# Kernel optimization log

Measured on AMD Instinct MI355X. Metric: run time of the kernel, lower is better.

The kernel has to match this reference:

```python
import jax, jax.numpy as jnp
import numpy as np

NUM_HEADS = 8  # matches init_kwargs

def setup_inputs() -> dict:
    key = jax.random.key(0)
    ks = jax.random.split(key, 5)
    b, n, c = 8, 4096, 512
    scale_in = 1.0 / np.sqrt(c)
    return {
        'x': jax.random.normal(ks[0], (b, n, c), jnp.float32),
        'wqkv_w': jax.random.normal(ks[1], (3 * c, c), jnp.float32) * scale_in,
        'wqkv_b': jax.random.normal(ks[2], (3 * c,), jnp.float32) * 0.02,
        'wp_w': jax.random.normal(ks[3], (c, c), jnp.float32) * scale_in,
        'wp_b': jax.random.normal(ks[4], (c,), jnp.float32) * 0.02,
    }

def reference(x, wqkv_w, wqkv_b, wp_w, wp_b):
    b, n, c = x.shape
    h = NUM_HEADS
    d = c // h
    # QKV projection (torch Linear: x @ W^T + b)
    qkv = x @ wqkv_w.T + wqkv_b                      # (b, n, 3c)
    qkv = jnp.transpose(qkv.reshape(b, n, 3, c), (2, 0, 1, 3))
    q, k, v = qkv[0], qkv[1], qkv[2]                 # each (b, n, c)
    # Faithful to original: reshape (b,n,h,d) -> (b,h,n,d) is a FLAT
    # reinterpretation (torch .reshape), not a transpose.
    q = q.reshape(b, n, h, d).reshape(b, h, n, d)
    k = k.reshape(b, n, h, d).reshape(b, h, n, d)
    v = v.reshape(b, n, h, d).reshape(b, h, n, d)
    # Channel (cross-covariance) attention: contract over tokens n.
    scores = jnp.einsum('bhnd,bhne->bhde', q, k) / jnp.sqrt(jnp.float32(d))
    weights = jax.nn.softmax(scores, axis=-1)        # softmax over head_dim
    y = jnp.einsum('bhde,bhme->bhdm', weights, v)    # (b, h, d, n)
    y = jnp.transpose(y, (0, 3, 1, 2)).reshape(b, n, c)
    return y @ wp_w.T + wp_b
```

## Files before the change

kernel.cpp:

```cpp
#include <hip/hip_runtime.h>

typedef short s16x8 __attribute__((ext_vector_type(8)));
typedef float f32x4 __attribute__((ext_vector_type(4)));
typedef unsigned short us;

__device__ inline us f2bf(float f){
    union{float f;unsigned u;} v{f};
    unsigned r = v.u + 0x7fff + ((v.u>>16)&1);
    return (us)(r>>16);
}
__device__ inline float bf2f(us h){
    union{unsigned u;float f;} v{(unsigned)h<<16};
    return v.f;
}

__device__ __forceinline__ void glds16(const us* g, us* l){
    __builtin_amdgcn_global_load_lds(
        (const __attribute__((address_space(1))) unsigned int*)(g),
        (__attribute__((address_space(3))) unsigned int*)(l), 16, 0, 0);
}

__global__ void cast_f32_bf16(const float* __restrict__ src, us* __restrict__ dst, int n4){
    int i = blockIdx.x*blockDim.x + threadIdx.x;
    if(i < n4){
        float4 f = ((const float4*)src)[i];
        ushort4 o;
        o.x = f2bf(f.x); o.y = f2bf(f.y); o.z = f2bf(f.z); o.w = f2bf(f.w);
        ((ushort4*)dst)[i] = o;
    }
}

template<int BF16OUT>
__launch_bounds__(256,2)
__global__ void gemm_bt(const us* __restrict__ A, const us* __restrict__ B,
                        const float* __restrict__ bias, void* __restrict__ Cv,
                        int M, int N, int K){
    __shared__ __attribute__((aligned(16))) us sA[128*32];
    __shared__ __attribute__((aligned(16))) us sB[128*32];
    int t = threadIdx.x;
    int bm = blockIdx.y, bn = blockIdx.x;
    int lane = t & 63, wave = t >> 6;
    int quad = lane >> 4, l15 = lane & 15;
    int wm = wave >> 1, wn = wave & 1;

    int srow = wave*32 + (lane>>2);
    int scol = (lane&3)*8;
    const us* Ag = A + (size_t)(bm*128 + srow)*K + scol;
    const us* Bg = B + (size_t)(bn*128 + srow)*K + scol;
    us* sAw = &sA[(wave*32)*32];
    us* sBw = &sB[(wave*32)*32];

    f32x4 acc[4][4];
    #pragma unroll
    for(int i=0;i<4;i++)
        #pragma unroll
        for(int j=0;j<4;j++) acc[i][j] = (f32x4){0.f,0.f,0.f,0.f};

    for(int k0=0; k0<K; k0+=32){
        glds16(Ag + k0,                sAw);
        glds16(Ag + (size_t)16*K + k0, sAw + 16*32);
        glds16(Bg + k0,                sBw);
        glds16(Bg + (size_t)16*K + k0, sBw + 16*32);
        __syncthreads();
        s16x8 af[4], bfr[4];
        #pragma unroll
        for(int i=0;i<4;i++) af[i]  = *(const s16x8*)&sA[(wm*64 + i*16 + l15)*32 + quad*8];
        #pragma unroll
        for(int j=0;j<4;j++) bfr[j] = *(const s16x8*)&sB[(wn*64 + j*16 + l15)*32 + quad*8];
        #pragma unroll
        for(int i=0;i<4;i++)
            #pragma unroll
            for(int j=0;j<4;j++)
                acc[i][j] = __builtin_amdgcn_mfma_f32_16x16x32_bf16(af[i], bfr[j], acc[i][j], 0,0,0);
        __syncthreads();
    }

    int row0 = bm*128 + wm*64;
    int col0 = bn*128 + wn*64;
    #pragma unroll
    for(int j=0;j<4;j++){
        int col = col0 + j*16 + l15;
        float bv = bias[col];
        #pragma unroll
        for(int i=0;i<4;i++){
            int rbase = row0 + i*16 + quad*4;
            #pragma unroll
            for(int r=0;r<4;r++){
                float v = acc[i][j][r] + bv;
                if(BF16OUT) ((us*)Cv)[(size_t)(rbase+r)*N + col] = f2bf(v);
                else        ((float*)Cv)[(size_t)(rbase+r)*N + col] = v;
            }
        }
    }
}

__launch_bounds__(256,2)
__global__ void attn_scores_mfma(const us* __restrict__ qkv, float* __restrict__ Sp){
    __shared__ __attribute__((aligned(16))) us sQt[64*64];
    __shared__ __attribute__((aligned(16))) us sKt[64*64];
    int t = threadIdx.x;
    int kb = blockIdx.x, head = blockIdx.y;
    int lane = t & 63, w = t >> 6;
    int quad = lane >> 4, l15 = lane & 15;

    f32x4 acc[4];
    #pragma unroll
    for(int j=0;j<4;j++) acc[j] = (f32x4){0.f,0.f,0.f,0.f};

    for(int chunk=0; chunk<8; chunk++){
        int r0 = head*512 + kb*64 + chunk*8;
        #pragma unroll
        for(int it=0; it<2; it++){
            int i = it*256 + t;
            int row8 = i>>6, l = i&63;
            int d0 = (l&7)*8;
            int off = ((row8 ^ (l&7))<<3) | (l>>3);
            const us* gq = qkv + (size_t)(r0+row8)*1536 + l*8;
            union{uint4 v; us s[8];} q, k;
            q.v = *(const uint4*)gq;
            k.v = *(const uint4*)(gq + 512);
            #pragma unroll
            for(int j=0;j<8;j++){
                sQt[(d0+j)*64 + off] = q.s[j];
                sKt[(d0+j)*64 + off] = k.s[j];
            }
        }
        __syncthreads();
        #pragma unroll
        for(int ks=0; ks<2; ks++){
            int d = w*16 + l15;
            int tb = ks*4 + quad;
            s16x8 af = *(const s16x8*)&sQt[d*64 + ((tb ^ (d>>3))<<3)];
            #pragma unroll
            for(int jt=0; jt<4; jt++){
                int e = jt*16 + l15;
                s16x8 bf = *(const s16x8*)&sKt[e*64 + ((tb ^ (e>>3))<<3)];
                acc[jt] = __builtin_amdgcn_mfma_f32_16x16x32_bf16(af, bf, acc[jt], 0,0,0);
            }
        }
        __syncthreads();
    }

    float* S = Sp + (size_t)(kb*64 + head)*4096;
    #pragma unroll
    for(int jt=0; jt<4; jt++){
        int e = jt*16 + l15;
        #pragma unroll
        for(int r=0; r<4; r++){
            int d = w*16 + quad*4 + r;
            S[d*64 + e] = acc[jt][r];
        }
    }
}

__global__ void softmax_fuse(const float* __restrict__ Sp, us* __restrict__ W){
    int head = blockIdx.x;
    int t = threadIdx.x;
    int d = t>>2, eg = (t&3)*16;
    float v[16];
    #pragma unroll
    for(int e=0;e<16;e++) v[e]=0.f;
    for(int kb=0; kb<8; kb++){
        const float* p = Sp + (size_t)(kb*64 + head)*4096 + d*64 + eg;
        #pragma unroll
        for(int e4=0;e4<4;e4++){
            float4 f = ((const float4*)p)[e4];
            v[e4*4+0]+=f.x; v[e4*4+1]+=f.y; v[e4*4+2]+=f.z; v[e4*4+3]+=f.w;
        }
    }
    float m = -1e30f;
    #pragma unroll
    for(int e=0;e<16;e++){ v[e] *= 0.125f; m = fmaxf(m, v[e]); }
    m = fmaxf(m, __shfl_xor(m, 1));
    m = fmaxf(m, __shfl_xor(m, 2));
    float s = 0.f;
    #pragma unroll
    for(int e=0;e<16;e++){ v[e] = __expf(v[e]-m); s += v[e]; }
    s += __shfl_xor(s, 1);
    s += __shfl_xor(s, 2);
    float inv = 1.f/s;
    union{uint4 u[2]; us h[16];} o;
    #pragma unroll
    for(int e=0;e<16;e++) o.h[e] = f2bf(v[e]*inv);
    uint4* wp = (uint4*)(W + (size_t)head*4096 + d*64 + eg);
    wp[0] = o.u[0]; wp[1] = o.u[1];
}

__launch_bounds__(256,2)
__global__ void attn_pv(const us* __restrict__ qkv, const us* __restrict__ W,
                        us* __restrict__ attn){
    const int LV = 72;
    __shared__ __attribute__((aligned(16))) us sV[128*72];
    __shared__ __attribute__((aligned(16))) us sW[64*72];
    int t = threadIdx.x;
    int head = blockIdx.y, chunk = blockIdx.x;
    int rbase = head*512;
    #pragma unroll
    for(int it=0; it<4; it++){
        int i = it*2048 + t*8;
        int tok = i>>6, e = i&63;
        int qrow = i>>9, ch = i&511;
        *(uint4*)&sV[tok*LV + e] = *(const uint4*)&qkv[(size_t)(rbase + chunk*16 + qrow)*1536 + 1024 + ch];
    }
    #pragma unroll
    for(int it=0; it<2; it++){
        int i = it*2048 + t*8;
        int dd = i>>6, e = i&63;
        *(uint4*)&sW[dd*LV + e] = *(const uint4*)&W[head*4096 + i];
    }
    __syncthreads();
    int lane = t&63, w = t>>6, quad = lane>>4, l15 = lane&15;
    f32x4 acc[2][4];
    #pragma unroll
    for(int i=0;i<2;i++)
        #pragma unroll
        for(int j=0;j<4;j++) acc[i][j] = (f32x4){0.f,0.f,0.f,0.f};
    #pragma unroll
    for(int ks=0; ks<2; ks++){
        int k0 = ks*32;
        s16x8 af[2], bfr[4];
        #pragma unroll
        for(int mt=0;mt<2;mt++) af[mt]  = *(const s16x8*)&sV[(w*32+mt*16+l15)*LV + k0 + quad*8];
        #pragma unroll
        for(int nt=0;nt<4;nt++) bfr[nt] = *(const s16x8*)&sW[(nt*16+l15)*LV + k0 + quad*8];
        #pragma unroll
        for(int mt=0;mt<2;mt++)
            #pragma unroll
            for(int nt=0;nt<4;nt++)
                acc[mt][nt] = __builtin_amdgcn_mfma_f32_16x16x32_bf16(af[mt], bfr[nt], acc[mt][nt],0,0,0);
    }
    int b = head>>3, h = head&7;
    #pragma unroll
    for(int mt=0;mt<2;mt++){
        int mg = chunk*128 + w*32 + mt*16 + quad*4;
        #pragma unroll
        for(int nt=0;nt<4;nt++){
            int d = nt*16 + l15;
            #pragma unroll
            for(int r=0;r<4;r++){
                attn[(size_t)(b*4096 + mg + r)*512 + h*64 + d] = f2bf(acc[mt][nt][r]);
            }
        }
    }
}

extern "C" void kernel_launch(void* const* d_in, const int* in_sizes, int n_in,
                              void* d_out, int out_size, void* d_ws, size_t ws_size,
                              hipStream_t stream){
    const float* x      = (const float*)d_in[0];
    const float* wqkv_w = (const float*)d_in[1];
    const float* wqkv_b = (const float*)d_in[2];
    const float* wp_w   = (const float*)d_in[3];
    const float* wp_b   = (const float*)d_in[4];

    char* ws = (char*)d_ws;
    us*    qkvbf  = (us*)(ws);
    us*    xbf    = (us*)(ws + 100663296);
    us*    attnbf = xbf;
    us*    wqkvbf = (us*)(ws + 134217728);
    us*    wpbf   = (us*)(ws + 135790592);
    float* Spart  = (float*)(ws + 136314880);
    us*    Wsm    = (us*)(ws + 144703488);

    cast_f32_bf16<<<16384,256,0,stream>>>(x,      xbf,    16777216/4);
    cast_f32_bf16<<<768,  256,0,stream>>>(wqkv_w, wqkvbf, 786432/4);
    cast_f32_bf16<<<256,  256,0,stream>>>(wp_w,   wpbf,   262144/4);

    gemm_bt<1><<<dim3(12,256),256,0,stream>>>(xbf, wqkvbf, wqkv_b, (void*)qkvbf, 32768,1536,512);

    attn_scores_mfma<<<dim3(8,64),256,0,stream>>>(qkvbf, Spart);
    softmax_fuse<<<64,256,0,stream>>>(Spart, Wsm);

    attn_pv<<<dim3(32,64),256,0,stream>>>(qkvbf, Wsm, attnbf);

    gemm_bt<0><<<dim3(4,256),256,0,stream>>>(attnbf, wpbf, wp_b, d_out, 32768,512,512);
}
```

Measured before the change: 271.2 us.

## Fuse x cast into QKV GEMM with LDS-resident A rows and register-streamed B

Replaces the tiled 128x128 GEMM with a kernel that loads a full 64x512 row strip of A into swizzled LDS once (converting fp32 x to bf16 in-kernel for the QKV projection) and then loops over all output column tiles. B fragments are read directly from global/L2 with register double buffering instead of through LDS. This removes the separate x cast kernel and its bf16 round trip, and cuts per-k-step barriers. The trade-off is 64KB of LDS per block, which lowers occupancy, plus uncoalesced-ish global B reads relying on cache, and only 512 blocks on the GPU.

```diff
diff --git a/kernel.cpp b/kernel.cpp
--- a/kernel.cpp
+++ b/kernel.cpp
@@ -30,65 +30,94 @@
     }
 }
 
-template<int BF16OUT>
+template<int CVT, int BF16OUT>
 __launch_bounds__(256,2)
-__global__ void gemm_bt(const us* __restrict__ A, const us* __restrict__ B,
-                        const float* __restrict__ bias, void* __restrict__ Cv,
-                        int M, int N, int K){
-    __shared__ __attribute__((aligned(16))) us sA[128*32];
-    __shared__ __attribute__((aligned(16))) us sB[128*32];
+__global__ void gemm_ares(const void* __restrict__ Av, const us* __restrict__ B,
+                          const float* __restrict__ bias, void* __restrict__ Cv,
+                          int N){
+    __shared__ __attribute__((aligned(16))) us sA[64*512];
     int t = threadIdx.x;
-    int bm = blockIdx.y, bn = blockIdx.x;
-    int lane = t & 63, wave = t >> 6;
-    int quad = lane >> 4, l15 = lane & 15;
-    int wm = wave >> 1, wn = wave & 1;
-
-    int srow = wave*32 + (lane>>2);
-    int scol = (lane&3)*8;
-    const us* Ag = A + (size_t)(bm*128 + srow)*K + scol;
-    const us* Bg = B + (size_t)(bn*128 + srow)*K + scol;
-    us* sAw = &sA[(wave*32)*32];
-    us* sBw = &sB[(wave*32)*32];
-
-    f32x4 acc[4][4];
-    #pragma unroll
-    for(int i=0;i<4;i++)
-        #pragma unroll
-        for(int j=0;j<4;j++) acc[i][j] = (f32x4){0.f,0.f,0.f,0.f};
-
-    for(int k0=0; k0<K; k0+=32){
-        glds16(Ag + k0,                sAw);
-        glds16(Ag + (size_t)16*K + k0, sAw + 16*32);
-        glds16(Bg + k0,                sBw);
-        glds16(Bg + (size_t)16*K + k0, sBw + 16*32);
-        __syncthreads();
-        s16x8 af[4], bfr[4];
-        #pragma unroll
-        for(int i=0;i<4;i++) af[i]  = *(const s16x8*)&sA[(wm*64 + i*16 + l15)*32 + quad*8];
-        #pragma unroll
-        for(int j=0;j<4;j++) bfr[j] = *(const s16x8*)&sB[(wn*64 + j*16 + l15)*32 + quad*8];
+    int bm = blockIdx.x;
+    int lane = t&63, w = t>>6;
+    int quad = lane>>4, l15 = lane&15;
+
+    if(CVT){
+        const float* A = (const float*)Av;
+        #pragma unroll
+        for(int it=0; it<16; it++){
+            int g = it*256 + t;
+            int r = g>>6, ck = g&63;
+            const float4* gp = (const float4*)(A + ((size_t)(bm*64+r)*512 + ck*8));
+            float4 f0 = gp[0], f1 = gp[1];
+            ushort4 h0, h1;
+            h0.x=f2bf(f0.x); h0.y=f2bf(f0.y); h0.z=f2bf(f0.z); h0.w=f2bf(f0.w);
+            h1.x=f2bf(f1.x); h1.y=f2bf(f1.y); h1.z=f2bf(f1.z); h1.w=f2bf(f1.w);
+            us* dst = &sA[(size_t)r*512 + (size_t)(ck ^ (r&7))*8];
+            *(ushort4*)dst = h0; *(ushort4*)(dst+4) = h1;
+        }
+    } else {
+        const us* A = (const us*)Av;
+        #pragma unroll
+        for(int it=0; it<16; it++){
+            int r0 = it*4 + w;
+            int ck = lane ^ (r0&7);
+            glds16(A + (size_t)(bm*64+r0)*512 + ck*8, &sA[(size_t)r0*512]);
+        }
+    }
+    __syncthreads();
+
+    for(int nt=0; nt<N; nt+=256){
+        int c0 = nt + w*64;
+        f32x4 acc[4][4];
         #pragma unroll
         for(int i=0;i<4;i++)
             #pragma unroll
-            for(int j=0;j<4;j++)
-                acc[i][j] = __builtin_amdgcn_mfma_f32_16x16x32_bf16(af[i], bfr[j], acc[i][j], 0,0,0);
-        __syncthreads();
-    }
-
-    int row0 = bm*128 + wm*64;
-    int col0 = bn*128 + wn*64;
-    #pragma unroll
-    for(int j=0;j<4;j++){
-        int col = col0 + j*16 + l15;
-        float bv = bias[col];
+            for(int j=0;j<4;j++) acc[i][j] = (f32x4){0.f,0.f,0.f,0.f};
+
+        s16x8 af[2][4], bf[2][4];
         #pragma unroll
         for(int i=0;i<4;i++){
-            int rbase = row0 + i*16 + quad*4;
-            #pragma unroll
-            for(int r=0;r<4;r++){
-                float v = acc[i][j][r] + bv;
-                if(BF16OUT) ((us*)Cv)[(size_t)(rbase+r)*N + col] = f2bf(v);
-                else        ((float*)Cv)[(size_t)(rbase+r)*N + col] = v;
+            int r = i*16 + l15;
+            af[0][i] = *(const s16x8*)&sA[(size_t)r*512 + (size_t)((quad ^ (r&7)))*8];
+        }
+        #pragma unroll
+        for(int j=0;j<4;j++)
+            bf[0][j] = *(const s16x8*)&B[(size_t)(c0 + j*16 + l15)*512 + quad*8];
+
+        #pragma unroll
+        for(int k=0;k<16;k++){
+            int cur = k&1, nx = cur^1;
+            if(k<15){
+                int kc = (k+1)*4 + quad;
+                #pragma unroll
+                for(int i=0;i<4;i++){
+                    int r = i*16 + l15;
+                    af[nx][i] = *(const s16x8*)&sA[(size_t)r*512 + (size_t)(kc ^ (r&7))*8];
+                }
+                #pragma unroll
+                for(int j=0;j<4;j++)
+                    bf[nx][j] = *(const s16x8*)&B[(size_t)(c0 + j*16 + l15)*512 + (k+1)*32 + quad*8];
+            }
+            #pragma unroll
+            for(int i=0;i<4;i++)
+                #pragma unroll
+                for(int j=0;j<4;j++)
+                    acc[i][j] = __builtin_amdgcn_mfma_f32_16x16x32_bf16(af[cur][i], bf[cur][j], acc[i][j], 0,0,0);
+        }
+
+        #pragma unroll
+        for(int j=0;j<4;j++){
+            int col = c0 + j*16 + l15;
+            float bv = bias[col];
+            #pragma unroll
+            for(int i=0;i<4;i++){
+                int row = bm*64 + i*16 + quad*4;
+                #pragma unroll
+                for(int r=0;r<4;r++){
+                    float v = acc[i][j][r] + bv;
+                    if(BF16OUT) ((us*)Cv)[(size_t)(row+r)*N + col] = f2bf(v);
+                    else        ((float*)Cv)[(size_t)(row+r)*N + col] = v;
+                }
             }
         }
     }
@@ -134,8 +163,8 @@
             #pragma unroll
             for(int jt=0; jt<4; jt++){
                 int e = jt*16 + l15;
-                s16x8 bf = *(const s16x8*)&sKt[e*64 + ((tb ^ (e>>3))<<3)];
-                acc[jt] = __builtin_amdgcn_mfma_f32_16x16x32_bf16(af, bf, acc[jt], 0,0,0);
+                s16x8 bfv = *(const s16x8*)&sKt[e*64 + ((tb ^ (e>>3))<<3)];
+                acc[jt] = __builtin_amdgcn_mfma_f32_16x16x32_bf16(af, bfv, acc[jt], 0,0,0);
             }
         }
         __syncthreads();
@@ -255,23 +284,21 @@
 
     char* ws = (char*)d_ws;
     us*    qkvbf  = (us*)(ws);
-    us*    xbf    = (us*)(ws + 100663296);
-    us*    attnbf = xbf;
+    us*    attnbf = (us*)(ws + 100663296);
     us*    wqkvbf = (us*)(ws + 134217728);
     us*    wpbf   = (us*)(ws + 135790592);
     float* Spart  = (float*)(ws + 136314880);
     us*    Wsm    = (us*)(ws + 144703488);
 
-    cast_f32_bf16<<<16384,256,0,stream>>>(x,      xbf,    16777216/4);
-    cast_f32_bf16<<<768,  256,0,stream>>>(wqkv_w, wqkvbf, 786432/4);
-    cast_f32_bf16<<<256,  256,0,stream>>>(wp_w,   wpbf,   262144/4);
-
-    gemm_bt<1><<<dim3(12,256),256,0,stream>>>(xbf, wqkvbf, wqkv_b, (void*)qkvbf, 32768,1536,512);
+    cast_f32_bf16<<<768, 256,0,stream>>>(wqkv_w, wqkvbf, 786432/4);
+    cast_f32_bf16<<<256, 256,0,stream>>>(wp_w,   wpbf,   262144/4);
+
+    gemm_ares<1,1><<<512,256,0,stream>>>((const void*)x, wqkvbf, wqkv_b, (void*)qkvbf, 1536);
 
     attn_scores_mfma<<<dim3(8,64),256,0,stream>>>(qkvbf, Spart);
     softmax_fuse<<<64,256,0,stream>>>(Spart, Wsm);
 
     attn_pv<<<dim3(32,64),256,0,stream>>>(qkvbf, Wsm, attnbf);
 
-    gemm_bt<0><<<dim3(4,256),256,0,stream>>>(attnbf, wpbf, wp_b, d_out, 32768,512,512);
-}
+    gemm_ares<0,0><<<512,256,0,stream>>>((const void*)attnbf, wpbf, wp_b, d_out, 512);
+}
```

New measurement: 406.3 us. 49.8% more time.

## Fold attention weights into output projection and fuse x cast into QKV GEMM

Applied to the files above, without the earlier changes.

The per-head softmax weights are multiplied into the output projection weights in advance (a small wpfold kernel), so the attention-value product and the output GEMM collapse into one GEMM that reads V straight from the qkv buffer. The x fp32-to-bf16 cast kernel is removed: the QKV GEMM loads fp32 x, converts it in registers and register-prefetches the next K slice. Both GEMMs now use a 1D grid remapped by XCD for L2 locality. This cuts the attn intermediate write/read, one kernel, and the separate x cast pass. In exchange it adds a per-batch fused weight matrix and rounds the folded weights to bf16 a second time.

```diff
diff --git a/kernel.cpp b/kernel.cpp
--- a/kernel.cpp
+++ b/kernel.cpp
@@ -30,24 +30,24 @@
     }
 }
 
-template<int BF16OUT>
 __launch_bounds__(256,2)
-__global__ void gemm_bt(const us* __restrict__ A, const us* __restrict__ B,
-                        const float* __restrict__ bias, void* __restrict__ Cv,
-                        int M, int N, int K){
+__global__ void gemm_qkv(const float* __restrict__ X, const us* __restrict__ B,
+                         const float* __restrict__ bias, us* __restrict__ C){
     __shared__ __attribute__((aligned(16))) us sA[128*32];
     __shared__ __attribute__((aligned(16))) us sB[128*32];
     int t = threadIdx.x;
-    int bm = blockIdx.y, bn = blockIdx.x;
-    int lane = t & 63, wave = t >> 6;
-    int quad = lane >> 4, l15 = lane & 15;
-    int wm = wave >> 1, wn = wave & 1;
-
-    int srow = wave*32 + (lane>>2);
-    int scol = (lane&3)*8;
-    const us* Ag = A + (size_t)(bm*128 + srow)*K + scol;
-    const us* Bg = B + (size_t)(bn*128 + srow)*K + scol;
-    us* sAw = &sA[(wave*32)*32];
+    int id = blockIdx.x;
+    int xcd = id & 7, s = id >> 3;
+    int nt = s % 12, mt = xcd*32 + s/12;
+    int lane = t&63, wave = t>>6, quad = lane>>4, l15 = lane&15;
+    int wm = wave>>1, wn = wave&1;
+
+    int srA = t>>1, scA = (t&1)*16;
+    const float* Ag = X + (size_t)(mt*128 + srA)*512 + scA;
+    us* sAd = &sA[srA*32 + scA];
+
+    int srB = wave*32 + (lane>>2), scB = (lane&3)*8;
+    const us* Bg = B + (size_t)(nt*128 + srB)*512 + scB;
     us* sBw = &sB[(wave*32)*32];
 
     f32x4 acc[4][4];
@@ -56,11 +56,23 @@
         #pragma unroll
         for(int j=0;j<4;j++) acc[i][j] = (f32x4){0.f,0.f,0.f,0.f};
 
-    for(int k0=0; k0<K; k0+=32){
-        glds16(Ag + k0,                sAw);
-        glds16(Ag + (size_t)16*K + k0, sAw + 16*32);
-        glds16(Bg + k0,                sBw);
-        glds16(Bg + (size_t)16*K + k0, sBw + 16*32);
+    float4 p0 = ((const float4*)Ag)[0], p1 = ((const float4*)Ag)[1],
+           p2 = ((const float4*)Ag)[2], p3 = ((const float4*)Ag)[3];
+
+    for(int ki=0; ki<16; ki++){
+        int k0 = ki*32;
+        glds16(Bg + k0,          sBw);
+        glds16(Bg + 16*512 + k0, sBw + 16*32);
+        union{uint4 u[2]; us h[16];} o;
+        o.h[0]=f2bf(p0.x); o.h[1]=f2bf(p0.y); o.h[2]=f2bf(p0.z); o.h[3]=f2bf(p0.w);
+        o.h[4]=f2bf(p1.x); o.h[5]=f2bf(p1.y); o.h[6]=f2bf(p1.z); o.h[7]=f2bf(p1.w);
+        o.h[8]=f2bf(p2.x); o.h[9]=f2bf(p2.y); o.h[10]=f2bf(p2.z); o.h[11]=f2bf(p2.w);
+        o.h[12]=f2bf(p3.x); o.h[13]=f2bf(p3.y); o.h[14]=f2bf(p3.z); o.h[15]=f2bf(p3.w);
+        *(uint4*)sAd = o.u[0]; *(uint4*)(sAd+8) = o.u[1];
+        if(ki<15){
+            const float4* nxt = (const float4*)(Ag + k0 + 32);
+            p0 = nxt[0]; p1 = nxt[1]; p2 = nxt[2]; p3 = nxt[3];
+        }
         __syncthreads();
         s16x8 af[4], bfr[4];
         #pragma unroll
@@ -75,8 +87,7 @@
         __syncthreads();
     }
 
-    int row0 = bm*128 + wm*64;
-    int col0 = bn*128 + wn*64;
+    int row0 = mt*128 + wm*64, col0 = nt*128 + wn*64;
     #pragma unroll
     for(int j=0;j<4;j++){
         int col = col0 + j*16 + l15;
@@ -85,11 +96,8 @@
         for(int i=0;i<4;i++){
             int rbase = row0 + i*16 + quad*4;
             #pragma unroll
-            for(int r=0;r<4;r++){
-                float v = acc[i][j][r] + bv;
-                if(BF16OUT) ((us*)Cv)[(size_t)(rbase+r)*N + col] = f2bf(v);
-                else        ((float*)Cv)[(size_t)(rbase+r)*N + col] = v;
-            }
+            for(int r=0;r<4;r++)
+                C[(size_t)(rbase+r)*1536 + col] = f2bf(acc[i][j][r] + bv);
         }
     }
 }
@@ -134,8 +142,8 @@
             #pragma unroll
             for(int jt=0; jt<4; jt++){
                 int e = jt*16 + l15;
-                s16x8 bf = *(const s16x8*)&sKt[e*64 + ((tb ^ (e>>3))<<3)];
-                acc[jt] = __builtin_amdgcn_mfma_f32_16x16x32_bf16(af, bf, acc[jt], 0,0,0);
+                s16x8 bfv = *(const s16x8*)&sKt[e*64 + ((tb ^ (e>>3))<<3)];
+                acc[jt] = __builtin_amdgcn_mfma_f32_16x16x32_bf16(af, bfv, acc[jt], 0,0,0);
             }
         }
         __syncthreads();
@@ -186,60 +194,106 @@
     wp[0] = o.u[0]; wp[1] = o.u[1];
 }
 
+__launch_bounds__(256,1)
+__global__ void wpfold(const us* __restrict__ wpbf, const us* __restrict__ W,
+                       us* __restrict__ Mcat){
+    __shared__ us sWt[64*72];
+    int t = threadIdx.x;
+    int head = blockIdx.x, b = head>>3, h = head&7;
+    int lane = t&63, w = t>>6, quad = lane>>4, l15 = lane&15;
+    #pragma unroll
+    for(int it=0; it<2; it++){
+        int idx = it*2048 + t*8;
+        int d = idx>>6, e0 = idx&63;
+        union{uint4 v; us s[8];} q;
+        q.v = *(const uint4*)&W[(size_t)head*4096 + idx];
+        #pragma unroll
+        for(int j=0;j<8;j++) sWt[(e0+j)*72 + d] = q.s[j];
+    }
+    __syncthreads();
+    #pragma unroll
+    for(int i=0;i<8;i++){
+        int nO = w*128 + i*16 + l15;
+        s16x8 af0 = *(const s16x8*)&wpbf[(size_t)nO*512 + h*64 + quad*8];
+        s16x8 af1 = *(const s16x8*)&wpbf[(size_t)nO*512 + h*64 + 32 + quad*8];
+        #pragma unroll
+        for(int j=0;j<4;j++){
+            s16x8 bf0 = *(const s16x8*)&sWt[(j*16+l15)*72 + quad*8];
+            s16x8 bf1 = *(const s16x8*)&sWt[(j*16+l15)*72 + 32 + quad*8];
+            f32x4 acc = (f32x4){0.f,0.f,0.f,0.f};
+            acc = __builtin_amdgcn_mfma_f32_16x16x32_bf16(af0, bf0, acc, 0,0,0);
+            acc = __builtin_amdgcn_mfma_f32_16x16x32_bf16(af1, bf1, acc, 0,0,0);
+            #pragma unroll
+            for(int r=0;r<4;r++){
+                int row = w*128 + i*16 + quad*4 + r;
+                Mcat[((size_t)(b*512 + row))*512 + h*64 + j*16 + l15] = f2bf(acc[r]);
+            }
+        }
+    }
+}
+
 __launch_bounds__(256,2)
-__global__ void attn_pv(const us* __restrict__ qkv, const us* __restrict__ W,
-                        us* __restrict__ attn){
-    const int LV = 72;
-    __shared__ __attribute__((aligned(16))) us sV[128*72];
-    __shared__ __attribute__((aligned(16))) us sW[64*72];
-    int t = threadIdx.x;
-    int head = blockIdx.y, chunk = blockIdx.x;
-    int rbase = head*512;
-    #pragma unroll
-    for(int it=0; it<4; it++){
-        int i = it*2048 + t*8;
-        int tok = i>>6, e = i&63;
-        int qrow = i>>9, ch = i&511;
-        *(uint4*)&sV[tok*LV + e] = *(const uint4*)&qkv[(size_t)(rbase + chunk*16 + qrow)*1536 + 1024 + ch];
-    }
-    #pragma unroll
-    for(int it=0; it<2; it++){
-        int i = it*2048 + t*8;
-        int dd = i>>6, e = i&63;
-        *(uint4*)&sW[dd*LV + e] = *(const uint4*)&W[head*4096 + i];
-    }
-    __syncthreads();
-    int lane = t&63, w = t>>6, quad = lane>>4, l15 = lane&15;
-    f32x4 acc[2][4];
-    #pragma unroll
-    for(int i=0;i<2;i++)
+__global__ void gemm_vout(const us* __restrict__ qkv, const us* __restrict__ Mcat,
+                          const float* __restrict__ bias, float* __restrict__ out){
+    __shared__ __attribute__((aligned(16))) us sA[128*32];
+    __shared__ __attribute__((aligned(16))) us sB[128*32];
+    int t = threadIdx.x;
+    int id = blockIdx.x;
+    int xcd = id & 7, s = id >> 3;
+    int nt = s & 3, mt = xcd*32 + (s>>2);
+    int b = mt>>5, mr = mt&31;
+    int lane = t&63, wave = t>>6, quad = lane>>4, l15 = lane&15;
+    int wm = wave>>1, wn = wave&1;
+
+    int r = wave*32 + (lane>>2);
+    int m = mr*128 + r;
+    const us* Abase = qkv + ((size_t)(8*b)*512 + (m>>3))*1536 + 1024 + (m&7)*64 + (lane&3)*8;
+    us* sAw = &sA[(wave*32)*32];
+
+    int srB = wave*32 + (lane>>2), scB = (lane&3)*8;
+    const us* Bg = Mcat + ((size_t)(b*512 + nt*128 + srB))*512 + scB;
+    us* sBw = &sB[(wave*32)*32];
+
+    f32x4 acc[4][4];
+    #pragma unroll
+    for(int i=0;i<4;i++)
         #pragma unroll
         for(int j=0;j<4;j++) acc[i][j] = (f32x4){0.f,0.f,0.f,0.f};
-    #pragma unroll
-    for(int ks=0; ks<2; ks++){
-        int k0 = ks*32;
-        s16x8 af[2], bfr[4];
-        #pragma unroll
-        for(int mt=0;mt<2;mt++) af[mt]  = *(const s16x8*)&sV[(w*32+mt*16+l15)*LV + k0 + quad*8];
-        #pragma unroll
-        for(int nt=0;nt<4;nt++) bfr[nt] = *(const s16x8*)&sW[(nt*16+l15)*LV + k0 + quad*8];
-        #pragma unroll
-        for(int mt=0;mt<2;mt++)
-            #pragma unroll
-            for(int nt=0;nt<4;nt++)
-                acc[mt][nt] = __builtin_amdgcn_mfma_f32_16x16x32_bf16(af[mt], bfr[nt], acc[mt][nt],0,0,0);
-    }
-    int b = head>>3, h = head&7;
-    #pragma unroll
-    for(int mt=0;mt<2;mt++){
-        int mg = chunk*128 + w*32 + mt*16 + quad*4;
-        #pragma unroll
-        for(int nt=0;nt<4;nt++){
-            int d = nt*16 + l15;
-            #pragma unroll
-            for(int r=0;r<4;r++){
-                attn[(size_t)(b*4096 + mg + r)*512 + h*64 + d] = f2bf(acc[mt][nt][r]);
-            }
+
+    for(int ki=0; ki<16; ki++){
+        int k0 = ki*32;
+        int h = k0>>6, e0 = k0&63;
+        const us* Ag = Abase + (size_t)h*512*1536 + e0;
+        glds16(Ag,            sAw);
+        glds16(Ag + 2*1536,   sAw + 16*32);
+        glds16(Bg + k0,           sBw);
+        glds16(Bg + 16*512 + k0,  sBw + 16*32);
+        __syncthreads();
+        s16x8 af[4], bfr[4];
+        #pragma unroll
+        for(int i=0;i<4;i++) af[i]  = *(const s16x8*)&sA[(wm*64 + i*16 + l15)*32 + quad*8];
+        #pragma unroll
+        for(int j=0;j<4;j++) bfr[j] = *(const s16x8*)&sB[(wn*64 + j*16 + l15)*32 + quad*8];
+        #pragma unroll
+        for(int i=0;i<4;i++)
+            #pragma unroll
+            for(int j=0;j<4;j++)
+                acc[i][j] = __builtin_amdgcn_mfma_f32_16x16x32_bf16(af[i], bfr[j], acc[i][j], 0,0,0);
+        __syncthreads();
+    }
+
+    int row0 = b*4096 + mr*128 + wm*64;
+    int col0 = nt*128 + wn*64;
+    #pragma unroll
+    for(int j=0;j<4;j++){
+        int col = col0 + j*16 + l15;
+        float bv = bias[col];
+        #pragma unroll
+        for(int i=0;i<4;i++){
+            int rbase = row0 + i*16 + quad*4;
+            #pragma unroll
+            for(int r2=0;r2<4;r2++)
+                out[(size_t)(rbase+r2)*512 + col] = acc[i][j][r2] + bv;
         }
     }
 }
@@ -255,23 +309,21 @@
 
     char* ws = (char*)d_ws;
     us*    qkvbf  = (us*)(ws);
-    us*    xbf    = (us*)(ws + 100663296);
-    us*    attnbf = xbf;
-    us*    wqkvbf = (us*)(ws + 134217728);
-    us*    wpbf   = (us*)(ws + 135790592);
-    float* Spart  = (float*)(ws + 136314880);
-    us*    Wsm    = (us*)(ws + 144703488);
-
-    cast_f32_bf16<<<16384,256,0,stream>>>(x,      xbf,    16777216/4);
-    cast_f32_bf16<<<768,  256,0,stream>>>(wqkv_w, wqkvbf, 786432/4);
-    cast_f32_bf16<<<256,  256,0,stream>>>(wp_w,   wpbf,   262144/4);
-
-    gemm_bt<1><<<dim3(12,256),256,0,stream>>>(xbf, wqkvbf, wqkv_b, (void*)qkvbf, 32768,1536,512);
+    float* Spart  = (float*)(ws + 100663296);
+    us*    Wsm    = (us*)(ws + 109051904);
+    us*    Mcat   = (us*)(ws + 109576192);
+    us*    wqkvbf = (us*)(ws + 113770496);
+    us*    wpbf   = (us*)(ws + 115343360);
+
+    cast_f32_bf16<<<768, 256,0,stream>>>(wqkv_w, wqkvbf, 786432/4);
+    cast_f32_bf16<<<256, 256,0,stream>>>(wp_w,   wpbf,   262144/4);
+
+    gemm_qkv<<<3072,256,0,stream>>>(x, wqkvbf, wqkv_b, qkvbf);
 
     attn_scores_mfma<<<dim3(8,64),256,0,stream>>>(qkvbf, Spart);
     softmax_fuse<<<64,256,0,stream>>>(Spart, Wsm);
 
-    attn_pv<<<dim3(32,64),256,0,stream>>>(qkvbf, Wsm, attnbf);
-
-    gemm_bt<0><<<dim3(4,256),256,0,stream>>>(attnbf, wpbf, wp_b, d_out, 32768,512,512);
-}
+    wpfold<<<64,256,0,stream>>>(wpbf, Wsm, Mcat);
+
+    gemm_vout<<<1024,256,0,stream>>>(qkvbf, Mcat, wp_b, (float*)d_out);
+}
```

New measurement: 275.4 us. Within noise of the previous version (+1.6%).
